# Performance work log

Hardware: AMD Instinct MI355X
Metric: run time of the kernel (lower is better)

## Reference

```python
import jax, jax.numpy as jnp
import numpy as np

DIM = 2048
HID = 4096          # multiple_of*ceil(int(2*6144/3)/256)
STATE = 128
HEADS = 64
GROUPS = 1
CONV = 4
CHUNK = 256
HEAD_DIM = HID // HEADS            # 64
CONV_DIM = HID + 2 * GROUPS * STATE  # 4352
D_IN = 2 * HID + 2 * GROUPS * STATE + HEADS  # 8512


def setup_inputs() -> dict:
    key = jax.random.key(0)
    ks = jax.random.split(key, 8)
    x = jax.random.normal(ks[0], (1, 4096, DIM), dtype=jnp.float32)
    in_proj_w = jax.random.normal(ks[1], (D_IN, DIM), jnp.float32) * (DIM ** -0.5)
    conv_w = jax.random.normal(ks[2], (CONV_DIM, CONV), jnp.float32) * (CONV ** -0.5)
    # dt_bias init: log(expm1(uniform(dt_min, dt_max)))
    dt_bias = jnp.log(jnp.expm1(jax.random.uniform(ks[3], (HEADS,), jnp.float32, 0.001, 0.1)))
    # A_log init: log(uniform(A_init_min, A_init_max))
    A_log = jnp.log(jax.random.uniform(ks[4], (HEADS,), jnp.float32, 1.0, 16.0))
    D = jnp.ones((HEADS,), jnp.float32)
    norm_w = jnp.ones((HID,), jnp.float32)
    out_proj_w = jax.random.normal(ks[5], (DIM, HID), jnp.float32) * (HID ** -0.5)
    return dict(x=x, in_proj_w=in_proj_w, conv_w=conv_w, dt_bias=dt_bias,
                A_log=A_log, D=D, norm_w=norm_w, out_proj_w=out_proj_w)


def _causal_conv1d_silu(xBC, w):
    # xBC: (b, s, c); w: (c, k) depthwise causal conv, then SiLU
    b, s, c = xBC.shape
    k = w.shape[1]
    xp = jnp.pad(xBC, ((0, 0), (k - 1, 0), (0, 0)))
    out = xp[:, 0:s, :] * w[:, 0]
    for i in range(1, k):
        out = out + xp[:, i:i + s, :] * w[:, i]
    return jax.nn.silu(out)


def _ssd_chunk_scan(x, dt, A, B, C, D, chunk):
    # x: (b,s,h,p), dt: (b,s,h) post-softplus, A: (h,) negative, B,C: (b,s,g,n)
    b, s, h, p = x.shape
    g, n = B.shape[2], B.shape[3]
    c = s // chunk
    Bh = jnp.repeat(B, h // g, axis=2).reshape(b, c, chunk, h, n)
    Ch = jnp.repeat(C, h // g, axis=2).reshape(b, c, chunk, h, n)
    xr = x.reshape(b, c, chunk, h, p)
    dtr = dt.reshape(b, c, chunk, h)
    dA = dtr * A                      # (b,c,l,h)
    dAc = jnp.cumsum(dA, axis=2)      # (b,c,l,h)
    # intra-chunk (diagonal blocks): decay[i,j] = exp(dAc[i]-dAc[j]) for i>=j
    seg = dAc[:, :, :, None, :] - dAc[:, :, None, :, :]   # (b,c,l,l,h)
    mask = jnp.tril(jnp.ones((chunk, chunk), bool))
    Lmat = jnp.where(mask[None, None, :, :, None], jnp.exp(seg), 0.0)
    xdt = xr * dtr[..., None]         # dt-scaled inputs
    y_diag = jnp.einsum('bclhn,bcshn,bclsh,bcshp->bclhp', Ch, Bh, Lmat, xdt)
    # per-chunk end states
    dA_last = dAc[:, :, -1:, :]                       # (b,c,1,h)
    decay_states = jnp.exp(dA_last - dAc)             # (b,c,l,h)
    states = jnp.einsum('bclhn,bclh,bclhp->bchpn', Bh, decay_states, xdt)
    # inter-chunk recurrence
    chunk_decay = jnp.exp(dA_last[:, :, 0, :])        # (b,c,h)
    def step(carry, inp):
        dec, st = inp
        new = carry * dec[:, :, None, None] + st
        return new, carry
    init = jnp.zeros((b, h, p, n), x.dtype)
    _, prev = jax.lax.scan(step, init,
                           (jnp.moveaxis(chunk_decay, 1, 0), jnp.moveaxis(states, 1, 0)))
    prev = jnp.moveaxis(prev, 0, 1)                   # (b,c,h,p,n) state entering each chunk
    y_off = jnp.einsum('bclhn,bclh,bchpn->bclhp', Ch, jnp.exp(dAc), prev)
    y = (y_diag + y_off).reshape(b, s, h, p)
    return y + x * D[None, None, :, None]


def reference(x, in_proj_w, conv_w, dt_bias, A_log, D, norm_w, out_proj_w):
    b, s, _ = x.shape
    zxbcdt = x @ in_proj_w.T                          # (b,s,D_IN)
    z = zxbcdt[..., :HID]
    xBC = zxbcdt[..., HID:HID + CONV_DIM]
    dt = zxbcdt[..., HID + CONV_DIM:]                 # (b,s,heads)
    xBC = _causal_conv1d_silu(xBC, conv_w)
    xh = xBC[..., :HID].reshape(b, s, HEADS, HEAD_DIM)
    B = xBC[..., HID:HID + GROUPS * STATE].reshape(b, s, GROUPS, STATE)
    C = xBC[..., HID + GROUPS * STATE:].reshape(b, s, GROUPS, STATE)
    A = -jnp.exp(A_log)
    dt = jax.nn.softplus(dt + dt_bias)                # dt_softplus=True with dt_bias
    y = _ssd_chunk_scan(xh, dt, A, B, C, D, CHUNK)
    y = y.reshape(b, s, HID)
    y = y * jax.nn.silu(z)                            # gated
    y = y * jax.lax.rsqrt(jnp.mean(y * y, axis=-1, keepdims=True) + 1e-5) * norm_w
    return y @ out_proj_w.T
```

## Files before the change

kernel.cpp:

```cpp
#include <hip/hip_runtime.h>
#include <cstdint>
#include <cstddef>

#define SEQ      4096
#define DIMIN    2048
#define HID      4096
#define STATE    128
#define HEADS    64
#define HEAD_DIM 64
#define CONV_DIM 4352
#define D_IN     8512
#define WROWS    8576
#define XBCD_N   4480
#define CHUNK    256
#define NCHUNK   16

typedef __attribute__((ext_vector_type(8))) short short8;
typedef __attribute__((ext_vector_type(4))) float floatx4;
typedef __attribute__((ext_vector_type(4))) int   intx4;

#define AS1 __attribute__((address_space(1)))
#define AS3 __attribute__((address_space(3)))
__device__ __forceinline__ void gload_lds16(const void* g, void* l) {
    __builtin_amdgcn_global_load_lds((const AS1 unsigned int*)g, (AS3 unsigned int*)l, 16, 0, 0);
}

__device__ __forceinline__ unsigned short f2bf(float f) {
    union { float f; unsigned int u; } v; v.f = f;
    unsigned int r = v.u + 0x7FFFu + ((v.u >> 16) & 1u);
    return (unsigned short)(r >> 16);
}
__device__ __forceinline__ float bf2f(unsigned short u) {
    union { unsigned int u; float f; } v; v.u = ((unsigned int)u) << 16;
    return v.f;
}
__device__ __forceinline__ short8 asv(intx4 x) {
    union { intx4 i; short8 s; } u; u.i = x; return u.s;
}

#define DSR(dst, ptr, off) \
    asm volatile("ds_read_b128 %0, %1 offset:" off : "=&v"(dst) : "v"(ptr))
#define SB0   __builtin_amdgcn_sched_barrier(0)
#define BAR   __builtin_amdgcn_s_barrier()
#define LGKM0 asm volatile("s_waitcnt lgkmcnt(0)" ::: "memory")
#define VMC4  asm volatile("s_waitcnt vmcnt(4)" ::: "memory")

__global__ void k_convert(const float* __restrict__ src, unsigned short* __restrict__ dst,
                          long n, long nsrc) {
    long i = (long)blockIdx.x * blockDim.x + threadIdx.x;
    if (i >= n) return;
    float v = (i < nsrc) ? src[i] : 0.f;
    dst[i] = f2bf(v);
}

#define GBM 256
#define GBN 256
#define GBK 64

template <int BF16OUT>
__global__ __launch_bounds__(512, 2) void k_gemm256(
    const unsigned short* __restrict__ A, const unsigned short* __restrict__ B,
    void* __restrict__ Cout, float* __restrict__ Cpart,
    int Kloop, int ldk, int Nvalid, int ldc,
    float* __restrict__ aux, int auxc0)
{
    __shared__ __attribute__((aligned(16))) unsigned short smem[4 * 16384];

    const int tid  = threadIdx.x;
    const int wid  = tid >> 6, lane = tid & 63;
    const int wm   = (wid >> 2) * 128;
    const int wn   = (wid & 3) * 64;

    const int nbx = gridDim.x, nby = gridDim.y;
    const int nwg = nbx * nby * (int)gridDim.z;
    int flat = ((int)blockIdx.z * nby + blockIdx.y) * nbx + blockIdx.x;
    int q = nwg >> 3, r = nwg & 7;
    int xcd = flat & 7, loc = flat >> 3;
    int f2 = (xcd < r ? xcd * (q + 1) : r * (q + 1) + (xcd - r) * q) + loc;
    int bz  = f2 / (nbx * nby);
    int rm2 = f2 - bz * nbx * nby;
    int bm  = rm2 / nbx;
    int bn  = rm2 % nbx;

    const unsigned short* Ag = A + (long)bm * GBM * ldk + (long)bz * Kloop;
    const unsigned short* Bg = B + (long)bn * GBN * ldk + (long)bz * Kloop;

    const int s_r  = lane >> 3;
    const int s_kg = (lane & 7) ^ s_r;

    const int lrow = lane & 15;
    const int gk   = lane >> 4;
    const int slot0 = gk ^ (lrow & 7);

    const int aIdx0 = (wm + lrow) * 64 + slot0 * 8;
    const int bIdx0 = (wn + lrow) * 64 + slot0 * 8;
    const AS3 unsigned short* sm3 = (const AS3 unsigned short*)smem;
    const AS3 unsigned short* pA0k0 = sm3 + aIdx0;
    const AS3 unsigned short* pA0k1 = sm3 + (aIdx0 ^ 32);
    const AS3 unsigned short* pA1k0 = sm3 + 32768 + aIdx0;
    const AS3 unsigned short* pA1k1 = sm3 + 32768 + (aIdx0 ^ 32);
    const AS3 unsigned short* pB0k0 = sm3 + 16384 + bIdx0;
    const AS3 unsigned short* pB0k1 = sm3 + 16384 + (bIdx0 ^ 32);
    const AS3 unsigned short* pB1k0 = sm3 + 49152 + bIdx0;
    const AS3 unsigned short* pB1k1 = sm3 + 49152 + (bIdx0 ^ 32);

    unsigned short* AdB0 = smem;
    unsigned short* BdB0 = smem + 16384;
    unsigned short* AdB1 = smem + 32768;
    unsigned short* BdB1 = smem + 49152;

    floatx4 acc[8][4];
#pragma unroll
    for (int i = 0; i < 8; ++i)
#pragma unroll
        for (int j = 0; j < 4; ++j) acc[i][j] = (floatx4){0.f, 0.f, 0.f, 0.f};

    auto STAGE = [&](unsigned short* Ad, unsigned short* Bd, int tt, int p) {
        long k0 = (long)tt * GBK;
        if (k0 + GBK > Kloop) k0 = 0;
        const int seg = p * 8 + wid;
        const long ro = (long)(seg * 8 + s_r) * ldk + k0 + s_kg * 8;
        gload_lds16(Ag + ro, Ad + seg * 512);
        gload_lds16(Bg + ro, Bd + seg * 512);
    };

#pragma unroll
    for (int p = 0; p < 4; ++p) STAGE(AdB0, BdB0, 0, p);
    STAGE(AdB1, BdB1, 1, 0);
    STAGE(AdB1, BdB1, 1, 1);
    VMC4;
    BAR;
    SB0;

    const int nk = Kloop / GBK;

    auto tile_step = [&](const AS3 unsigned short* pAk0, const AS3 unsigned short* pAk1,
                         const AS3 unsigned short* pBk0, const AS3 unsigned short* pBk1,
                         unsigned short* AdC, unsigned short* BdC,
                         unsigned short* AdN, unsigned short* BdN, int t) {
        intx4 aL[4][2], aH[4][2], bV[4][2];
        DSR(aL[0][0], pAk0, "0");     DSR(aL[0][1], pAk1, "0");
        DSR(aL[1][0], pAk0, "2048");  DSR(aL[1][1], pAk1, "2048");
        DSR(aL[2][0], pAk0, "4096");  DSR(aL[2][1], pAk1, "4096");
        DSR(aL[3][0], pAk0, "6144");  DSR(aL[3][1], pAk1, "6144");
        DSR(bV[0][0], pBk0, "0");     DSR(bV[0][1], pBk1, "0");
        DSR(bV[1][0], pBk0, "2048");  DSR(bV[1][1], pBk1, "2048");
        STAGE(AdN, BdN, t + 1, 2);
        SB0; BAR; LGKM0; SB0;
        __builtin_amdgcn_s_setprio(1);
#pragma unroll
        for (int m = 0; m < 4; ++m)
#pragma unroll
            for (int n = 0; n < 2; ++n)
#pragma unroll
                for (int ks = 0; ks < 2; ++ks)
                    acc[m][n] = __builtin_amdgcn_mfma_f32_16x16x32_bf16(asv(aL[m][ks]), asv(bV[n][ks]), acc[m][n], 0, 0, 0);
        __builtin_amdgcn_s_setprio(0);
        SB0; BAR;
        DSR(bV[2][0], pBk0, "4096");  DSR(bV[2][1], pBk1, "4096");
        DSR(bV[3][0], pBk0, "6144");  DSR(bV[3][1], pBk1, "6144");
        STAGE(AdN, BdN, t + 1, 3);
        SB0; BAR; LGKM0; SB0;
        __builtin_amdgcn_s_setprio(1);
#pragma unroll
        for (int m = 0; m < 4; ++m)
#pragma unroll
            for (int n = 2; n < 4; ++n)
#pragma unroll
                for (int ks = 0; ks < 2; ++ks)
                    acc[m][n] = __builtin_amdgcn_mfma_f32_16x16x32_bf16(asv(aL[m][ks]), asv(bV[n][ks]), acc[m][n], 0, 0, 0);
        __builtin_amdgcn_s_setprio(0);
        SB0; BAR;
        DSR(aH[0][0], pAk0, "8192");  DSR(aH[0][1], pAk1, "8192");
        DSR(aH[1][0], pAk0, "10240"); DSR(aH[1][1], pAk1, "10240");
        DSR(aH[2][0], pAk0, "12288"); DSR(aH[2][1], pAk1, "12288");
        DSR(aH[3][0], pAk0, "14336"); DSR(aH[3][1], pAk1, "14336");
        STAGE(AdC, BdC, t + 2, 0);
        SB0; BAR; LGKM0; SB0;
        __builtin_amdgcn_s_setprio(1);
#pragma unroll
        for (int m = 0; m < 4; ++m)
#pragma unroll
            for (int n = 2; n < 4; ++n)
#pragma unroll
                for (int ks = 0; ks < 2; ++ks)
                    acc[m + 4][n] = __builtin_amdgcn_mfma_f32_16x16x32_bf16(asv(aH[m][ks]), asv(bV[n][ks]), acc[m + 4][n], 0, 0, 0);
        __builtin_amdgcn_s_setprio(0);
        SB0; BAR;
        STAGE(AdC, BdC, t + 2, 1);
        SB0; BAR; SB0;
        __builtin_amdgcn_s_setprio(1);
#pragma unroll
        for (int m = 0; m < 4; ++m)
#pragma unroll
            for (int n = 0; n < 2; ++n)
#pragma unroll
                for (int ks = 0; ks < 2; ++ks)
                    acc[m + 4][n] = __builtin_amdgcn_mfma_f32_16x16x32_bf16(asv(aH[m][ks]), asv(bV[n][ks]), acc[m + 4][n], 0, 0, 0);
        __builtin_amdgcn_s_setprio(0);
        VMC4; SB0; BAR;
    };

#pragma unroll 1
    for (int t = 0; t < nk; t += 2) {
        tile_step(pA0k0, pA0k1, pB0k0, pB0k1, AdB0, BdB0, AdB1, BdB1, t);
        tile_step(pA1k0, pA1k1, pB1k0, pB1k1, AdB1, BdB1, AdB0, BdB0, t + 1);
    }

    const int rcol = lane & 15, rrow = (lane >> 4) * 4;
#pragma unroll
    for (int m = 0; m < 8; ++m)
#pragma unroll
        for (int n = 0; n < 4; ++n) {
            const int colb = bn * GBN + wn + n * 16;
            if (colb >= Nvalid) continue;
            const int col = colb + rcol;
#pragma unroll
            for (int r2 = 0; r2 < 4; ++r2) {
                const int row = bm * GBM + wm + m * 16 + rrow + r2;
                float v = acc[m][n][r2];
                if (BF16OUT) {
                    ((unsigned short*)Cout)[(long)row * ldc + col] = f2bf(v);
                    if (aux && col >= auxc0 && col < auxc0 + 64)
                        aux[(long)row * 64 + (col - auxc0)] = v;
                } else {
                    float* op = bz ? Cpart : (float*)Cout;
                    op[(long)row * ldc + col] = v;
                }
            }
        }
}

__global__ void k_add(float* __restrict__ dst, const float* __restrict__ src, long n4) {
    long i = (long)blockIdx.x * blockDim.x + threadIdx.x;
    if (i >= n4) return;
    float4 a = ((const float4*)src)[i];
    float4 d = ((float4*)dst)[i];
    d.x += a.x; d.y += a.y; d.z += a.z; d.w += a.w;
    ((float4*)dst)[i] = d;
}

__global__ void k_conv(const unsigned short* __restrict__ xbcd, const float* __restrict__ convw,
                       unsigned short* __restrict__ xc) {
    long i = (long)blockIdx.x * 256 + threadIdx.x;
    if (i >= (long)SEQ * CONV_DIM) return;
    int c = (int)(i % CONV_DIM);
    int s = (int)(i / CONV_DIM);
    float w0 = convw[c * 4 + 0], w1 = convw[c * 4 + 1];
    float w2 = convw[c * 4 + 2], w3 = convw[c * 4 + 3];
    float acc = bf2f(xbcd[(long)s * XBCD_N + c]) * w3;
    if (s >= 1) acc += bf2f(xbcd[(long)(s - 1) * XBCD_N + c]) * w2;
    if (s >= 2) acc += bf2f(xbcd[(long)(s - 2) * XBCD_N + c]) * w1;
    if (s >= 3) acc += bf2f(xbcd[(long)(s - 3) * XBCD_N + c]) * w0;
    float sl = acc / (1.f + __expf(-acc));
    xc[i] = f2bf(sl);
}

__global__ __launch_bounds__(256) void k_dt(const float* __restrict__ dtraw,
        const float* __restrict__ dt_bias, const float* __restrict__ A_log,
        float* __restrict__ dtv, float* __restrict__ dAc, float* __restrict__ dAlast)
{
    int c = blockIdx.x, h = blockIdx.y;
    int l = threadIdx.x;
    __shared__ float sh[CHUNK];
    float v = dtraw[(long)(c * CHUNK + l) * 64 + h] + dt_bias[h];
    float dt = (v > 20.f) ? v : log1pf(__expf(v));
    float Ah = -__expf(A_log[h]);
    float dA = dt * Ah;
    sh[l] = dA;
    __syncthreads();
    float x = dA;
#pragma unroll
    for (int off = 1; off < CHUNK; off <<= 1) {
        float t = (l >= off) ? sh[l - off] : 0.f;
        __syncthreads();
        x += t;
        sh[l] = x;
        __syncthreads();
    }
    dtv[(long)(c * CHUNK + l) * HEADS + h] = dt;
    dAc[(long)(c * CHUNK + l) * HEADS + h] = x;
    if (l == CHUNK - 1) dAlast[c * HEADS + h] = x;
}

__global__ __launch_bounds__(256) void k_G(const unsigned short* __restrict__ xc, float* __restrict__ G) {
    int c = blockIdx.x, l = blockIdx.y;
    int s = threadIdx.x;
    __shared__ float Csh[STATE];
    if (s < STATE) Csh[s] = bf2f(xc[(long)(c * CHUNK + l) * CONV_DIM + HID + STATE + s]);
    __syncthreads();
    const unsigned short* Brow = xc + (long)(c * CHUNK + s) * CONV_DIM + HID;
    float acc = 0.f;
#pragma unroll
    for (int n = 0; n < STATE; n += 8) {
        short8 b8 = *(const short8*)&Brow[n];
#pragma unroll
        for (int j = 0; j < 8; ++j)
            acc += Csh[n + j] * bf2f((unsigned short)b8[j]);
    }
    G[((long)c * CHUNK + l) * CHUNK + s] = acc;
}

__global__ __launch_bounds__(256) void k_states(
    const unsigned short* __restrict__ xc, const float* __restrict__ dtv,
    const float* __restrict__ dAc, const float* __restrict__ dAlast,
    float* __restrict__ states)
{
    int c = blockIdx.x, h = blockIdx.y;
    int t = threadIdx.x;
    __shared__ float xs[64][64];
    __shared__ float dA_sh[CHUNK], dt_sh[CHUNK];
    long base_s = (long)c * CHUNK;
    dA_sh[t] = dAc[(base_s + t) * HEADS + h];
    dt_sh[t] = dtv[(base_s + t) * HEADS + h];
    __syncthreads();
    float dAl = dAlast[c * HEADS + h];
    int p0 = t >> 5;
    int n0 = t & 31;
    float acc[8][4];
#pragma unroll
    for (int ip = 0; ip < 8; ++ip)
#pragma unroll
        for (int j = 0; j < 4; ++j) acc[ip][j] = 0.f;

    for (int lb = 0; lb < 4; ++lb) {
#pragma unroll
        for (int i = 0; i < 16; ++i) {
            int e = t + i * 256;
            int r = e >> 6, pcol = e & 63;
            float ds = __expf(dAl - dA_sh[lb * 64 + r]) * dt_sh[lb * 64 + r];
            xs[r][pcol] = bf2f(xc[(base_s + lb * 64 + r) * CONV_DIM + h * HEAD_DIM + pcol]) * ds;
        }
        __syncthreads();
        for (int lp = 0; lp < 64; ++lp) {
            const unsigned short* Brow = xc + (base_s + lb * 64 + lp) * CONV_DIM + HID;
            float bv[4];
#pragma unroll
            for (int j = 0; j < 4; ++j) bv[j] = bf2f(Brow[n0 + 32 * j]);
#pragma unroll
            for (int ip = 0; ip < 8; ++ip) {
                float xv = xs[lp][p0 + 8 * ip];
#pragma unroll
                for (int j = 0; j < 4; ++j) acc[ip][j] += xv * bv[j];
            }
        }
        __syncthreads();
    }
    float* Sb = states + (long)(c * HEADS + h) * HEAD_DIM * STATE;
#pragma unroll
    for (int ip = 0; ip < 8; ++ip)
#pragma unroll
        for (int j = 0; j < 4; ++j)
            Sb[(p0 + 8 * ip) * STATE + n0 + 32 * j] = acc[ip][j];
}

__global__ void k_scan(float* __restrict__ states, const float* __restrict__ dAlast) {
    int t = blockIdx.x * 256 + threadIdx.x;
    if (t >= HEADS * HEAD_DIM * STATE) return;
    int h = t >> 13;
    const long stride = (long)HEADS * HEAD_DIM * STATE;
    float carry = 0.f;
    for (int c = 0; c < NCHUNK; ++c) {
        float s = states[c * stride + t];
        float dec = __expf(dAlast[c * HEADS + h]);
        states[c * stride + t] = carry;
        carry = carry * dec + s;
    }
}

#define XDTS 264
#define PVS  136
__global__ __launch_bounds__(256, 3) void k_ssd_y(
    const unsigned short* __restrict__ xc, const float* __restrict__ G,
    const float* __restrict__ dtv, const float* __restrict__ dAc,
    const float* __restrict__ prev, const float* __restrict__ Dp,
    unsigned short* __restrict__ y)
{
    __shared__ __attribute__((aligned(16))) unsigned short xdtT[64 * XDTS];
    __shared__ __attribute__((aligned(16))) unsigned short pvB[64 * PVS];
    __shared__ float dA_sh[CHUNK];
    __shared__ float dt_sh[CHUNK];
    const int c = blockIdx.x, h = blockIdx.y;
    const int t = threadIdx.x;
    const int w = t >> 6, lane = t & 63;
    const long base_s = (long)c * CHUNK;

    dA_sh[t] = dAc[(base_s + t) * HEADS + h];
    dt_sh[t] = dtv[(base_s + t) * HEADS + h];
    __syncthreads();

    {
        const float* Pb = prev + (long)(c * HEADS + h) * HEAD_DIM * STATE;
#pragma unroll
        for (int i = 0; i < 32; ++i) {
            int e = t + i * 256;
            int p = e >> 7, n = e & 127;
            pvB[p * PVS + n] = f2bf(Pb[e]);
        }
    }
#pragma unroll
    for (int i = 0; i < 64; ++i) {
        int e = t + i * 256;
        int p = e & 63, s = e >> 6;
        float v = bf2f(xc[(base_s + s) * CONV_DIM + h * HEAD_DIM + p]) * dt_sh[s];
        xdtT[p * XDTS + s] = f2bf(v);
    }
    __syncthreads();

    floatx4 acc[4][4];
#pragma unroll
    for (int i = 0; i < 4; ++i)
#pragma unroll
        for (int j = 0; j < 4; ++j) acc[i][j] = (floatx4){0.f, 0.f, 0.f, 0.f};

    const int lrow = lane & 15;
    const int kgrp = (lane >> 4) * 8;
    float myA[4], eAl[4];
#pragma unroll
    for (int i = 0; i < 4; ++i) {
        int l = w * 64 + i * 16 + lrow;
        myA[i] = dA_sh[l];
        eAl[i] = __expf(myA[i]);
    }

    for (int k0 = 0; k0 < STATE; k0 += 32) {
        short8 af[4], bfr[4];
#pragma unroll
        for (int i = 0; i < 4; ++i) {
            int l = w * 64 + i * 16 + lrow;
            union { short8 v; unsigned short u[8]; } r, o;
            r.v = *(const short8*)&xc[(base_s + l) * CONV_DIM + (HID + STATE) + k0 + kgrp];
#pragma unroll
            for (int j = 0; j < 8; ++j) o.u[j] = f2bf(bf2f(r.u[j]) * eAl[i]);
            af[i] = o.v;
        }
#pragma unroll
        for (int j = 0; j < 4; ++j)
            bfr[j] = *(const short8*)&pvB[(j * 16 + lrow) * PVS + k0 + kgrp];
#pragma unroll
        for (int i = 0; i < 4; ++i)
#pragma unroll
            for (int j = 0; j < 4; ++j)
                acc[i][j] = __builtin_amdgcn_mfma_f32_16x16x32_bf16(af[i], bfr[j], acc[i][j], 0, 0, 0);
    }

    for (int k0 = 0; k0 < (w + 1) * 64; k0 += 32) {
        short8 af[4], bfr[4];
#pragma unroll
        for (int i = 0; i < 4; ++i) {
            int l = w * 64 + i * 16 + lrow;
            const float* Gp = G + (base_s + l) * (long)CHUNK + k0 + kgrp;
            float4 g0 = *(const float4*)Gp;
            float4 g1 = *(const float4*)(Gp + 4);
            float ga[8] = {g0.x, g0.y, g0.z, g0.w, g1.x, g1.y, g1.z, g1.w};
            union { short8 v; unsigned short u[8]; } o;
#pragma unroll
            for (int j = 0; j < 8; ++j) {
                int s = k0 + kgrp + j;
                float e = __expf(fminf(myA[i] - dA_sh[s], 0.f));
                float m = (s <= l) ? ga[j] * e : 0.f;
                o.u[j] = f2bf(m);
            }
            af[i] = o.v;
        }
#pragma unroll
        for (int j = 0; j < 4; ++j)
            bfr[j] = *(const short8*)&xdtT[(j * 16 + lrow) * XDTS + k0 + kgrp];
#pragma unroll
        for (int i = 0; i < 4; ++i)
#pragma unroll
            for (int j = 0; j < 4; ++j)
                acc[i][j] = __builtin_amdgcn_mfma_f32_16x16x32_bf16(af[i], bfr[j], acc[i][j], 0, 0, 0);
    }

    const float Dh = Dp[h];
    const int rrow = (lane >> 4) * 4;
#pragma unroll
    for (int i = 0; i < 4; ++i)
#pragma unroll
        for (int j = 0; j < 4; ++j) {
            int p = j * 16 + lrow;
#pragma unroll
            for (int r = 0; r < 4; ++r) {
                int l = w * 64 + i * 16 + rrow + r;
                float v = acc[i][j][r] + Dh * bf2f(xc[(base_s + l) * CONV_DIM + h * HEAD_DIM + p]);
                y[(base_s + l) * (long)HID + h * HEAD_DIM + p] = f2bf(v);
            }
        }
}

__global__ __launch_bounds__(256) void k_norm(
    const unsigned short* __restrict__ y, const unsigned short* __restrict__ z,
    const float* __restrict__ norm_w, unsigned short* __restrict__ yb)
{
    int s = blockIdx.x;
    int t = threadIdx.x;
    const unsigned short* yrow = y + (long)s * HID;
    const unsigned short* zrow = z + (long)s * HID;
    float vals[16];
    float ss = 0.f;
#pragma unroll
    for (int i = 0; i < 16; ++i) {
        int j = t + i * 256;
        float yv = bf2f(yrow[j]);
        float zv = bf2f(zrow[j]);
        float g = yv * (zv / (1.f + __expf(-zv)));
        vals[i] = g;
        ss += g * g;
    }
#pragma unroll
    for (int off = 32; off > 0; off >>= 1) ss += __shfl_down(ss, off);
    __shared__ float wsum[4];
    int lane = t & 63, wid = t >> 6;
    if (lane == 0) wsum[wid] = ss;
    __syncthreads();
    float total = wsum[0] + wsum[1] + wsum[2] + wsum[3];
    float scale = rsqrtf(total / HID + 1e-5f);
#pragma unroll
    for (int i = 0; i < 16; ++i) {
        int j = t + i * 256;
        yb[(long)s * HID + j] = f2bf(vals[i] * scale * norm_w[j]);
    }
}

extern "C" void kernel_launch(void* const* d_in, const int* in_sizes, int n_in,
                              void* d_out, int out_size, void* d_ws, size_t ws_size,
                              hipStream_t stream) {
    const float* x          = (const float*)d_in[0];
    const float* in_proj_w  = (const float*)d_in[1];
    const float* conv_w     = (const float*)d_in[2];
    const float* dt_bias    = (const float*)d_in[3];
    const float* A_log      = (const float*)d_in[4];
    const float* Dp         = (const float*)d_in[5];
    const float* norm_w     = (const float*)d_in[6];
    const float* out_proj_w = (const float*)d_in[7];
    char* ws = (char*)d_ws;

    const size_t off_xb    = 0;
    const size_t off_wbin  = off_xb    + (size_t)SEQ * DIMIN * 2;
    const size_t off_xbcd  = off_wbin  + (size_t)WROWS * DIMIN * 2;
    const size_t off_xc    = off_xbcd  + (size_t)SEQ * XBCD_N * 2;
    const size_t off_dtraw = off_xc    + (size_t)SEQ * CONV_DIM * 2;
    const size_t off_dtv   = off_dtraw + (size_t)SEQ * 64 * 4;
    const size_t off_dAc   = off_dtv   + (size_t)SEQ * HEADS * 4;
    const size_t off_dAl   = off_dAc   + (size_t)SEQ * HEADS * 4;
    const size_t off_G     = off_dAl   + (size_t)NCHUNK * HEADS * 4;
    const size_t needed    = off_G     + (size_t)NCHUNK * CHUNK * CHUNK * 4;
    if (ws_size < needed) return;

    unsigned short* xb    = (unsigned short*)(ws + off_xb);
    unsigned short* wbin  = (unsigned short*)(ws + off_wbin);
    unsigned short* xbcd  = (unsigned short*)(ws + off_xbcd);
    unsigned short* xc    = (unsigned short*)(ws + off_xc);
    float* dtraw = (float*)(ws + off_dtraw);
    float* dtv   = (float*)(ws + off_dtv);
    float* dAc   = (float*)(ws + off_dAc);
    float* dAl   = (float*)(ws + off_dAl);
    float* G     = (float*)(ws + off_G);

    float* states      = (float*)d_out;
    unsigned short* z  = (unsigned short*)d_out;
    unsigned short* y  = xbcd;
    unsigned short* yb = xc;
    unsigned short* wob = wbin;
    float* gpart = (float*)(ws + off_xbcd);

    { long n = (long)SEQ * DIMIN;
      k_convert<<<(unsigned)((n + 255) / 256), 256, 0, stream>>>(x, xb, n, n); }
    { long n = (long)WROWS * DIMIN, nsrc = (long)D_IN * DIMIN;
      k_convert<<<(unsigned)((n + 255) / 256), 256, 0, stream>>>(in_proj_w, wbin, n, nsrc); }
    k_gemm256<1><<<dim3((XBCD_N + GBN - 1) / GBN, SEQ / GBM, 1), 512, 0, stream>>>(
        xb, wbin + (size_t)HID * DIMIN, (void*)xbcd, nullptr,
        DIMIN, DIMIN, XBCD_N, XBCD_N, dtraw, 4352);
    { long n = (long)SEQ * CONV_DIM;
      k_conv<<<(unsigned)((n + 255) / 256), 256, 0, stream>>>(xbcd, conv_w, xc); }
    k_dt<<<dim3(NCHUNK, HEADS), 256, 0, stream>>>(dtraw, dt_bias, A_log, dtv, dAc, dAl);
    k_G<<<dim3(NCHUNK, CHUNK), 256, 0, stream>>>(xc, G);
    k_states<<<dim3(NCHUNK, HEADS), 256, 0, stream>>>(xc, dtv, dAc, dAl, states);
    k_scan<<<(HEADS * HEAD_DIM * STATE) / 256, 256, 0, stream>>>(states, dAl);
    k_ssd_y<<<dim3(NCHUNK, HEADS), 256, 0, stream>>>(xc, G, dtv, dAc, states, Dp, y);
    k_gemm256<1><<<dim3(HID / GBN, SEQ / GBM, 1), 512, 0, stream>>>(
        xb, wbin, (void*)z, nullptr, DIMIN, DIMIN, HID, HID, nullptr, 0);
    k_norm<<<SEQ, 256, 0, stream>>>(y, z, norm_w, yb);
    { long n = (long)DIMIN * HID;
      k_convert<<<(unsigned)((n + 255) / 256), 256, 0, stream>>>(out_proj_w, wob, n, n); }
    k_gemm256<0><<<dim3(DIMIN / GBN, SEQ / GBM, 2), 512, 0, stream>>>(
        yb, wob, d_out, gpart, HID / 2, HID, DIMIN, DIMIN, nullptr, 0);
    k_add<<<(unsigned)(((long)SEQ * DIMIN / 4 + 255) / 256), 256, 0, stream>>>(
        (float*)d_out, gpart, (long)SEQ * DIMIN / 4);
}
```

Measured before the change: 726.1 us.

## Restructure GEMM main loop with register prefetch and fewer barriers

Rewrites the 256x256 bf16 GEMM inner loop. The first A/B fragments of the next K-tile are now prefetched into registers while the last MFMA group of the current tile runs. Partial lgkmcnt waits replace full waits so MFMAs can start before all LDS reads land. The four split global->LDS stage calls per tile are merged into one bulk stage issued once per tile, which drops several block barriers per step. This aims to cut barrier stalls and LDS latency exposure, at the cost of more live registers and a coarser global-load schedule.

Measured after the change: 727.3 us. No clear change (+0.2%).

```diff
diff --git a/kernel.cpp b/kernel.cpp
--- a/kernel.cpp
+++ b/kernel.cpp
@@ -42,8 +42,10 @@
     asm volatile("ds_read_b128 %0, %1 offset:" off : "=&v"(dst) : "v"(ptr))
 #define SB0   __builtin_amdgcn_sched_barrier(0)
 #define BAR   __builtin_amdgcn_s_barrier()
+#define LGKM8 asm volatile("s_waitcnt lgkmcnt(8)" ::: "memory")
+#define LGKM4 asm volatile("s_waitcnt lgkmcnt(4)" ::: "memory")
 #define LGKM0 asm volatile("s_waitcnt lgkmcnt(0)" ::: "memory")
-#define VMC4  asm volatile("s_waitcnt vmcnt(4)" ::: "memory")
+#define VMC8  asm volatile("s_waitcnt vmcnt(8)" ::: "memory")
 
 __global__ void k_convert(const float* __restrict__ src, unsigned short* __restrict__ dst,
                           long n, long nsrc) {
@@ -115,96 +117,124 @@
 #pragma unroll
         for (int j = 0; j < 4; ++j) acc[i][j] = (floatx4){0.f, 0.f, 0.f, 0.f};
 
-    auto STAGE = [&](unsigned short* Ad, unsigned short* Bd, int tt, int p) {
+    auto STAGEALL = [&](unsigned short* Ad, unsigned short* Bd, int tt) {
         long k0 = (long)tt * GBK;
         if (k0 + GBK > Kloop) k0 = 0;
-        const int seg = p * 8 + wid;
-        const long ro = (long)(seg * 8 + s_r) * ldk + k0 + s_kg * 8;
-        gload_lds16(Ag + ro, Ad + seg * 512);
-        gload_lds16(Bg + ro, Bd + seg * 512);
+#pragma unroll
+        for (int p = 0; p < 4; ++p) {
+            const int seg = p * 8 + wid;
+            const long ro = (long)(seg * 8 + s_r) * ldk + k0 + s_kg * 8;
+            gload_lds16(Ag + ro, Ad + seg * 512);
+            gload_lds16(Bg + ro, Bd + seg * 512);
+        }
     };
 
-#pragma unroll
-    for (int p = 0; p < 4; ++p) STAGE(AdB0, BdB0, 0, p);
-    STAGE(AdB1, BdB1, 1, 0);
-    STAGE(AdB1, BdB1, 1, 1);
-    VMC4;
-    BAR;
+    intx4 aL01A[2][2], b01A[2][2], aL01B[2][2], b01B[2][2];
+
+    STAGEALL(AdB0, BdB0, 0);
+    STAGEALL(AdB1, BdB1, 1);
+    VMC8; SB0; BAR; SB0;
+    DSR(aL01A[0][0], pA0k0, "0");     DSR(aL01A[0][1], pA0k1, "0");
+    DSR(aL01A[1][0], pA0k0, "2048");  DSR(aL01A[1][1], pA0k1, "2048");
+    DSR(b01A[0][0],  pB0k0, "0");     DSR(b01A[0][1],  pB0k1, "0");
+    DSR(b01A[1][0],  pB0k0, "2048");  DSR(b01A[1][1],  pB0k1, "2048");
     SB0;
 
     const int nk = Kloop / GBK;
 
-    auto tile_step = [&](const AS3 unsigned short* pAk0, const AS3 unsigned short* pAk1,
+    auto tile_step = [&](intx4 (&hAL)[2][2], intx4 (&hB)[2][2],
+                         intx4 (&nAL)[2][2], intx4 (&nB)[2][2],
+                         const AS3 unsigned short* pAk0, const AS3 unsigned short* pAk1,
                          const AS3 unsigned short* pBk0, const AS3 unsigned short* pBk1,
-                         unsigned short* AdC, unsigned short* BdC,
-                         unsigned short* AdN, unsigned short* BdN, int t) {
-        intx4 aL[4][2], aH[4][2], bV[4][2];
-        DSR(aL[0][0], pAk0, "0");     DSR(aL[0][1], pAk1, "0");
-        DSR(aL[1][0], pAk0, "2048");  DSR(aL[1][1], pAk1, "2048");
-        DSR(aL[2][0], pAk0, "4096");  DSR(aL[2][1], pAk1, "4096");
-        DSR(aL[3][0], pAk0, "6144");  DSR(aL[3][1], pAk1, "6144");
-        DSR(bV[0][0], pBk0, "0");     DSR(bV[0][1], pBk1, "0");
-        DSR(bV[1][0], pBk0, "2048");  DSR(bV[1][1], pBk1, "2048");
-        STAGE(AdN, BdN, t + 1, 2);
-        SB0; BAR; LGKM0; SB0;
+                         const AS3 unsigned short* qAk0, const AS3 unsigned short* qAk1,
+                         const AS3 unsigned short* qBk0, const AS3 unsigned short* qBk1,
+                         unsigned short* AdC, unsigned short* BdC, int t) {
+        intx4 aL23[2][2], b23[2][2], aH[4][2];
+        DSR(aL23[0][0], pAk0, "4096");  DSR(aL23[0][1], pAk1, "4096");
+        DSR(aL23[1][0], pAk0, "6144");  DSR(aL23[1][1], pAk1, "6144");
+        DSR(b23[0][0],  pBk0, "4096");  DSR(b23[0][1],  pBk1, "4096");
+        DSR(b23[1][0],  pBk0, "6144");  DSR(b23[1][1],  pBk1, "6144");
+        SB0; LGKM8; SB0;
         __builtin_amdgcn_s_setprio(1);
 #pragma unroll
+        for (int m = 0; m < 2; ++m)
+#pragma unroll
+            for (int n = 0; n < 2; ++n)
+#pragma unroll
+                for (int ks = 0; ks < 2; ++ks)
+                    acc[m][n] = __builtin_amdgcn_mfma_f32_16x16x32_bf16(asv(hAL[m][ks]), asv(hB[n][ks]), acc[m][n], 0, 0, 0);
+        __builtin_amdgcn_s_setprio(0);
+        SB0; LGKM4; SB0;
+        __builtin_amdgcn_s_setprio(1);
+#pragma unroll
+        for (int m = 0; m < 2; ++m)
+#pragma unroll
+            for (int n = 0; n < 2; ++n)
+#pragma unroll
+                for (int ks = 0; ks < 2; ++ks)
+                    acc[2 + m][n] = __builtin_amdgcn_mfma_f32_16x16x32_bf16(asv(aL23[m][ks]), asv(hB[n][ks]), acc[2 + m][n], 0, 0, 0);
+        __builtin_amdgcn_s_setprio(0);
+        DSR(aH[0][0], pAk0, "8192");   DSR(aH[0][1], pAk1, "8192");
+        DSR(aH[1][0], pAk0, "10240");  DSR(aH[1][1], pAk1, "10240");
+        DSR(aH[2][0], pAk0, "12288");  DSR(aH[2][1], pAk1, "12288");
+        DSR(aH[3][0], pAk0, "14336");  DSR(aH[3][1], pAk1, "14336");
+        SB0; LGKM8; SB0;
+        __builtin_amdgcn_s_setprio(1);
+#pragma unroll
+        for (int m = 0; m < 2; ++m)
+#pragma unroll
+            for (int n = 2; n < 4; ++n)
+#pragma unroll
+                for (int ks = 0; ks < 2; ++ks)
+                    acc[m][n] = __builtin_amdgcn_mfma_f32_16x16x32_bf16(asv(hAL[m][ks]), asv(b23[n - 2][ks]), acc[m][n], 0, 0, 0);
+#pragma unroll
+        for (int m = 0; m < 2; ++m)
+#pragma unroll
+            for (int n = 2; n < 4; ++n)
+#pragma unroll
+                for (int ks = 0; ks < 2; ++ks)
+                    acc[2 + m][n] = __builtin_amdgcn_mfma_f32_16x16x32_bf16(asv(aL23[m][ks]), asv(b23[n - 2][ks]), acc[2 + m][n], 0, 0, 0);
+        __builtin_amdgcn_s_setprio(0);
+        SB0; LGKM0; SB0;
+        __builtin_amdgcn_s_setprio(1);
+#pragma unroll
         for (int m = 0; m < 4; ++m)
 #pragma unroll
-            for (int n = 0; n < 2; ++n)
+            for (int n = 2; n < 4; ++n)
 #pragma unroll
                 for (int ks = 0; ks < 2; ++ks)
-                    acc[m][n] = __builtin_amdgcn_mfma_f32_16x16x32_bf16(asv(aL[m][ks]), asv(bV[n][ks]), acc[m][n], 0, 0, 0);
+                    acc[4 + m][n] = __builtin_amdgcn_mfma_f32_16x16x32_bf16(asv(aH[m][ks]), asv(b23[n - 2][ks]), acc[4 + m][n], 0, 0, 0);
         __builtin_amdgcn_s_setprio(0);
         SB0; BAR;
-        DSR(bV[2][0], pBk0, "4096");  DSR(bV[2][1], pBk1, "4096");
-        DSR(bV[3][0], pBk0, "6144");  DSR(bV[3][1], pBk1, "6144");
-        STAGE(AdN, BdN, t + 1, 3);
-        SB0; BAR; LGKM0; SB0;
+        STAGEALL(AdC, BdC, t + 2);
+        SB0; VMC8; SB0; BAR; SB0;
+        DSR(nAL[0][0], qAk0, "0");     DSR(nAL[0][1], qAk1, "0");
+        DSR(nAL[1][0], qAk0, "2048");  DSR(nAL[1][1], qAk1, "2048");
+        DSR(nB[0][0],  qBk0, "0");     DSR(nB[0][1],  qBk1, "0");
+        DSR(nB[1][0],  qBk0, "2048");  DSR(nB[1][1],  qBk1, "2048");
+        SB0;
         __builtin_amdgcn_s_setprio(1);
 #pragma unroll
         for (int m = 0; m < 4; ++m)
 #pragma unroll
-            for (int n = 2; n < 4; ++n)
+            for (int n = 0; n < 2; ++n)
 #pragma unroll
                 for (int ks = 0; ks < 2; ++ks)
-                    acc[m][n] = __builtin_amdgcn_mfma_f32_16x16x32_bf16(asv(aL[m][ks]), asv(bV[n][ks]), acc[m][n], 0, 0, 0);
+                    acc[4 + m][n] = __builtin_amdgcn_mfma_f32_16x16x32_bf16(asv(aH[m][ks]), asv(hB[n][ks]), acc[4 + m][n], 0, 0, 0);
         __builtin_amdgcn_s_setprio(0);
-        SB0; BAR;
-        DSR(aH[0][0], pAk0, "8192");  DSR(aH[0][1], pAk1, "8192");
-        DSR(aH[1][0], pAk0, "10240"); DSR(aH[1][1], pAk1, "10240");
-        DSR(aH[2][0], pAk0, "12288"); DSR(aH[2][1], pAk1, "12288");
-        DSR(aH[3][0], pAk0, "14336"); DSR(aH[3][1], pAk1, "14336");
-        STAGE(AdC, BdC, t + 2, 0);
-        SB0; BAR; LGKM0; SB0;
-        __builtin_amdgcn_s_setprio(1);
-#pragma unroll
-        for (int m = 0; m < 4; ++m)
-#pragma unroll
-            for (int n = 2; n < 4; ++n)
-#pragma unroll
-                for (int ks = 0; ks < 2; ++ks)
-                    acc[m + 4][n] = __builtin_amdgcn_mfma_f32_16x16x32_bf16(asv(aH[m][ks]), asv(bV[n][ks]), acc[m + 4][n], 0, 0, 0);
-        __builtin_amdgcn_s_setprio(0);
-        SB0; BAR;
-        STAGE(AdC, BdC, t + 2, 1);
-        SB0; BAR; SB0;
-        __builtin_amdgcn_s_setprio(1);
-#pragma unroll
-        for (int m = 0; m < 4; ++m)
-#pragma unroll
-            for (int n = 0; n < 2; ++n)
-#pragma unroll
-                for (int ks = 0; ks < 2; ++ks)
-                    acc[m + 4][n] = __builtin_amdgcn_mfma_f32_16x16x32_bf16(asv(aH[m][ks]), asv(bV[n][ks]), acc[m + 4][n], 0, 0, 0);
-        __builtin_amdgcn_s_setprio(0);
-        VMC4; SB0; BAR;
+        SB0;
     };
 
 #pragma unroll 1
     for (int t = 0; t < nk; t += 2) {
-        tile_step(pA0k0, pA0k1, pB0k0, pB0k1, AdB0, BdB0, AdB1, BdB1, t);
-        tile_step(pA1k0, pA1k1, pB1k0, pB1k1, AdB1, BdB1, AdB0, BdB0, t + 1);
+        tile_step(aL01A, b01A, aL01B, b01B,
+                  pA0k0, pA0k1, pB0k0, pB0k1,
+                  pA1k0, pA1k1, pB1k0, pB1k1,
+                  AdB0, BdB0, t);
+        tile_step(aL01B, b01B, aL01A, b01A,
+                  pA1k0, pA1k1, pB1k0, pB1k1,
+                  pA0k0, pA0k1, pB0k0, pB0k1,
+                  AdB1, BdB1, t + 1);
     }
 
     const int rcol = lane & 15, rrow = (lane >> 4) * 4;
```

## Shrink GEMM tile to 128x256x32 with triple-buffered single-barrier pipeline

Applied to the files above, without the earlier changes.

Replaces the 256x256x64 double-buffered GEMM with a 128x256 tile, K-step 32, and a three-buffer LDS ring, which allows four workgroups per CU and needs one barrier per K step. The aim is higher occupancy and fewer barrier stalls, at the cost of lower arithmetic intensity per tile and more global traffic. The host launch grid is not shown changing for the new GBM, so correctness depends on the unseen launch code using GBM.

Result: slower. 748.7 us (+3.1%).

```diff
diff --git a/kernel.cpp b/kernel.cpp
--- a/kernel.cpp
+++ b/kernel.cpp
@@ -43,7 +43,7 @@
 #define SB0   __builtin_amdgcn_sched_barrier(0)
 #define BAR   __builtin_amdgcn_s_barrier()
 #define LGKM0 asm volatile("s_waitcnt lgkmcnt(0)" ::: "memory")
-#define VMC4  asm volatile("s_waitcnt vmcnt(4)" ::: "memory")
+#define VMC3  asm volatile("s_waitcnt vmcnt(3)" ::: "memory")
 
 __global__ void k_convert(const float* __restrict__ src, unsigned short* __restrict__ dst,
                           long n, long nsrc) {
@@ -53,22 +53,22 @@
     dst[i] = f2bf(v);
 }
 
-#define GBM 256
+#define GBM 128
 #define GBN 256
-#define GBK 64
+#define GBK 32
 
 template <int BF16OUT>
-__global__ __launch_bounds__(512, 2) void k_gemm256(
+__global__ __launch_bounds__(512, 4) void k_gemm256(
     const unsigned short* __restrict__ A, const unsigned short* __restrict__ B,
     void* __restrict__ Cout, float* __restrict__ Cpart,
     int Kloop, int ldk, int Nvalid, int ldc,
     float* __restrict__ aux, int auxc0)
 {
-    __shared__ __attribute__((aligned(16))) unsigned short smem[4 * 16384];
+    __shared__ __attribute__((aligned(16))) unsigned short smem[3 * 12288];
 
     const int tid  = threadIdx.x;
     const int wid  = tid >> 6, lane = tid & 63;
-    const int wm   = (wid >> 2) * 128;
+    const int wm   = (wid >> 2) * 64;
     const int wn   = (wid & 3) * 64;
 
     const int nbx = gridDim.x, nby = gridDim.y;
@@ -85,131 +85,76 @@
     const unsigned short* Ag = A + (long)bm * GBM * ldk + (long)bz * Kloop;
     const unsigned short* Bg = B + (long)bn * GBN * ldk + (long)bz * Kloop;
 
-    const int s_r  = lane >> 3;
-    const int s_kg = (lane & 7) ^ s_r;
+    const int s_r  = lane >> 2;
+    const int s_kg = (lane & 3) ^ ((lane >> 2) & 3) ^ ((lane >> 4) & 3);
 
     const int lrow = lane & 15;
     const int gk   = lane >> 4;
-    const int slot0 = gk ^ (lrow & 7);
-
-    const int aIdx0 = (wm + lrow) * 64 + slot0 * 8;
-    const int bIdx0 = (wn + lrow) * 64 + slot0 * 8;
+    const int slot0 = gk ^ (lrow & 3) ^ ((lrow >> 2) & 3);
+
+    const int aIdx = (wm + lrow) * 32 + slot0 * 8;
+    const int bIdx = (wn + lrow) * 32 + slot0 * 8;
+
     const AS3 unsigned short* sm3 = (const AS3 unsigned short*)smem;
-    const AS3 unsigned short* pA0k0 = sm3 + aIdx0;
-    const AS3 unsigned short* pA0k1 = sm3 + (aIdx0 ^ 32);
-    const AS3 unsigned short* pA1k0 = sm3 + 32768 + aIdx0;
-    const AS3 unsigned short* pA1k1 = sm3 + 32768 + (aIdx0 ^ 32);
-    const AS3 unsigned short* pB0k0 = sm3 + 16384 + bIdx0;
-    const AS3 unsigned short* pB0k1 = sm3 + 16384 + (bIdx0 ^ 32);
-    const AS3 unsigned short* pB1k0 = sm3 + 49152 + bIdx0;
-    const AS3 unsigned short* pB1k1 = sm3 + 49152 + (bIdx0 ^ 32);
-
-    unsigned short* AdB0 = smem;
-    unsigned short* BdB0 = smem + 16384;
-    unsigned short* AdB1 = smem + 32768;
-    unsigned short* BdB1 = smem + 49152;
-
-    floatx4 acc[8][4];
-#pragma unroll
-    for (int i = 0; i < 8; ++i)
+    const AS3 unsigned short* rA0 = sm3 + aIdx;
+    const AS3 unsigned short* rB0 = sm3 + 4096 + bIdx;
+    const AS3 unsigned short* rA1 = sm3 + 12288 + aIdx;
+    const AS3 unsigned short* rB1 = sm3 + 12288 + 4096 + bIdx;
+    const AS3 unsigned short* rA2 = sm3 + 24576 + aIdx;
+    const AS3 unsigned short* rB2 = sm3 + 24576 + 4096 + bIdx;
+
+    unsigned short* d0 = smem;
+    unsigned short* d1 = smem + 12288;
+    unsigned short* d2 = smem + 24576;
+
+    floatx4 acc[4][4];
+#pragma unroll
+    for (int i = 0; i < 4; ++i)
 #pragma unroll
         for (int j = 0; j < 4; ++j) acc[i][j] = (floatx4){0.f, 0.f, 0.f, 0.f};
 
-    auto STAGE = [&](unsigned short* Ad, unsigned short* Bd, int tt, int p) {
+    auto STAGE = [&](unsigned short* buf, int tt) {
         long k0 = (long)tt * GBK;
         if (k0 + GBK > Kloop) k0 = 0;
-        const int seg = p * 8 + wid;
-        const long ro = (long)(seg * 8 + s_r) * ldk + k0 + s_kg * 8;
-        gload_lds16(Ag + ro, Ad + seg * 512);
-        gload_lds16(Bg + ro, Bd + seg * 512);
+        gload_lds16(Ag + (long)(wid * 16 + s_r) * ldk + k0 + s_kg * 8, buf + wid * 512);
+        gload_lds16(Bg + (long)(wid * 16 + s_r) * ldk + k0 + s_kg * 8, buf + 4096 + wid * 512);
+        gload_lds16(Bg + (long)((8 + wid) * 16 + s_r) * ldk + k0 + s_kg * 8, buf + 4096 + (8 + wid) * 512);
     };
 
-#pragma unroll
-    for (int p = 0; p < 4; ++p) STAGE(AdB0, BdB0, 0, p);
-    STAGE(AdB1, BdB1, 1, 0);
-    STAGE(AdB1, BdB1, 1, 1);
-    VMC4;
-    BAR;
-    SB0;
+    STAGE(d0, 0);
+    STAGE(d1, 1);
+    VMC3;
+    BAR; SB0;
 
     const int nk = Kloop / GBK;
 
-    auto tile_step = [&](const AS3 unsigned short* pAk0, const AS3 unsigned short* pAk1,
-                         const AS3 unsigned short* pBk0, const AS3 unsigned short* pBk1,
-                         unsigned short* AdC, unsigned short* BdC,
-                         unsigned short* AdN, unsigned short* BdN, int t) {
-        intx4 aL[4][2], aH[4][2], bV[4][2];
-        DSR(aL[0][0], pAk0, "0");     DSR(aL[0][1], pAk1, "0");
-        DSR(aL[1][0], pAk0, "2048");  DSR(aL[1][1], pAk1, "2048");
-        DSR(aL[2][0], pAk0, "4096");  DSR(aL[2][1], pAk1, "4096");
-        DSR(aL[3][0], pAk0, "6144");  DSR(aL[3][1], pAk1, "6144");
-        DSR(bV[0][0], pBk0, "0");     DSR(bV[0][1], pBk1, "0");
-        DSR(bV[1][0], pBk0, "2048");  DSR(bV[1][1], pBk1, "2048");
-        STAGE(AdN, BdN, t + 1, 2);
-        SB0; BAR; LGKM0; SB0;
+#pragma unroll 1
+    for (int t = 0; t < nk; ++t) {
+        STAGE(d2, t + 2);
+        intx4 aF[4], bF[4];
+        DSR(aF[0], rA0, "0");    DSR(aF[1], rA0, "1024");
+        DSR(aF[2], rA0, "2048"); DSR(aF[3], rA0, "3072");
+        DSR(bF[0], rB0, "0");    DSR(bF[1], rB0, "1024");
+        DSR(bF[2], rB0, "2048"); DSR(bF[3], rB0, "3072");
+        SB0; LGKM0; SB0;
         __builtin_amdgcn_s_setprio(1);
 #pragma unroll
         for (int m = 0; m < 4; ++m)
 #pragma unroll
-            for (int n = 0; n < 2; ++n)
-#pragma unroll
-                for (int ks = 0; ks < 2; ++ks)
-                    acc[m][n] = __builtin_amdgcn_mfma_f32_16x16x32_bf16(asv(aL[m][ks]), asv(bV[n][ks]), acc[m][n], 0, 0, 0);
+            for (int n = 0; n < 4; ++n)
+                acc[m][n] = __builtin_amdgcn_mfma_f32_16x16x32_bf16(asv(aF[m]), asv(bF[n]), acc[m][n], 0, 0, 0);
         __builtin_amdgcn_s_setprio(0);
-        SB0; BAR;
-        DSR(bV[2][0], pBk0, "4096");  DSR(bV[2][1], pBk1, "4096");
-        DSR(bV[3][0], pBk0, "6144");  DSR(bV[3][1], pBk1, "6144");
-        STAGE(AdN, BdN, t + 1, 3);
-        SB0; BAR; LGKM0; SB0;
-        __builtin_amdgcn_s_setprio(1);
-#pragma unroll
-        for (int m = 0; m < 4; ++m)
-#pragma unroll
-            for (int n = 2; n < 4; ++n)
-#pragma unroll
-                for (int ks = 0; ks < 2; ++ks)
-                    acc[m][n] = __builtin_amdgcn_mfma_f32_16x16x32_bf16(asv(aL[m][ks]), asv(bV[n][ks]), acc[m][n], 0, 0, 0);
-        __builtin_amdgcn_s_setprio(0);
-        SB0; BAR;
-        DSR(aH[0][0], pAk0, "8192");  DSR(aH[0][1], pAk1, "8192");
-        DSR(aH[1][0], pAk0, "10240"); DSR(aH[1][1], pAk1, "10240");
-        DSR(aH[2][0], pAk0, "12288"); DSR(aH[2][1], pAk1, "12288");
-        DSR(aH[3][0], pAk0, "14336"); DSR(aH[3][1], pAk1, "14336");
-        STAGE(AdC, BdC, t + 2, 0);
-        SB0; BAR; LGKM0; SB0;
-        __builtin_amdgcn_s_setprio(1);
-#pragma unroll
-        for (int m = 0; m < 4; ++m)
-#pragma unroll
-            for (int n = 2; n < 4; ++n)
-#pragma unroll
-                for (int ks = 0; ks < 2; ++ks)
-                    acc[m + 4][n] = __builtin_amdgcn_mfma_f32_16x16x32_bf16(asv(aH[m][ks]), asv(bV[n][ks]), acc[m + 4][n], 0, 0, 0);
-        __builtin_amdgcn_s_setprio(0);
-        SB0; BAR;
-        STAGE(AdC, BdC, t + 2, 1);
+        SB0;
+        VMC3;
         SB0; BAR; SB0;
-        __builtin_amdgcn_s_setprio(1);
-#pragma unroll
-        for (int m = 0; m < 4; ++m)
-#pragma unroll
-            for (int n = 0; n < 2; ++n)
-#pragma unroll
-                for (int ks = 0; ks < 2; ++ks)
-                    acc[m + 4][n] = __builtin_amdgcn_mfma_f32_16x16x32_bf16(asv(aH[m][ks]), asv(bV[n][ks]), acc[m + 4][n], 0, 0, 0);
-        __builtin_amdgcn_s_setprio(0);
-        VMC4; SB0; BAR;
-    };
-
-#pragma unroll 1
-    for (int t = 0; t < nk; t += 2) {
-        tile_step(pA0k0, pA0k1, pB0k0, pB0k1, AdB0, BdB0, AdB1, BdB1, t);
-        tile_step(pA1k0, pA1k1, pB1k0, pB1k1, AdB1, BdB1, AdB0, BdB0, t + 1);
+        const AS3 unsigned short* tA = rA0; rA0 = rA1; rA1 = rA2; rA2 = tA;
+        const AS3 unsigned short* tB = rB0; rB0 = rB1; rB1 = rB2; rB2 = tB;
+        unsigned short* td = d0; d0 = d1; d1 = d2; d2 = td;
     }
 
     const int rcol = lane & 15, rrow = (lane >> 4) * 4;
 #pragma unroll
-    for (int m = 0; m < 8; ++m)
+    for (int m = 0; m < 4; ++m)
 #pragma unroll
         for (int n = 0; n < 4; ++n) {
             const int colb = bn * GBN + wn + n * 16;
```
